# Kernel tuning notes

Measured on AMD Instinct MI355X. Metric: run time of the kernel, lower is better.

The kernel has to match this reference:

```python
import jax, jax.numpy as jnp
import numpy as np

N = 50000      # num nodes
E = 800000     # num edges
DIN = 64       # in_channels
H = 128        # hidden_channels
L = 3          # num GCN layers


def setup_inputs() -> dict:
    key = jax.random.key(0)
    ks = jax.random.split(key, 18)
    x = jax.random.normal(ks[0], (N, DIN), jnp.float32)
    edge_index = jax.random.randint(ks[1], (2, E), 0, N, dtype=jnp.int32)
    s_in = 1.0 / np.sqrt(DIN)
    s_h = 1.0 / np.sqrt(H)
    W_in = jax.random.normal(ks[2], (DIN, H), jnp.float32) * s_in
    b_in = jnp.zeros((H,), jnp.float32)
    Wc = jax.random.normal(ks[3], (L, H, H), jnp.float32) * s_h
    bc = jnp.zeros((L, H), jnp.float32)
    gamma = 1.0 + 0.1 * jax.random.normal(ks[4], (L, H), jnp.float32)
    beta = 0.1 * jax.random.normal(ks[5], (L, H), jnp.float32)
    rmean = 0.1 * jax.random.normal(ks[6], (L, H), jnp.float32)
    rvar = jax.random.uniform(ks[7], (L, H), jnp.float32, 0.5, 1.5)
    W1 = jax.random.normal(ks[8], (H, H // 2), jnp.float32) * s_h
    b1 = jnp.zeros((H // 2,), jnp.float32)
    W2 = jax.random.normal(ks[9], (H // 2, 1), jnp.float32) * (1.0 / np.sqrt(H // 2))
    b2 = jnp.zeros((1,), jnp.float32)
    return dict(x=x, edge_index=edge_index, W_in=W_in, b_in=b_in, Wc=Wc, bc=bc,
                gamma=gamma, beta=beta, rmean=rmean, rvar=rvar,
                W1=W1, b1=b1, W2=W2, b2=b2)


def reference(x, edge_index, W_in, b_in, Wc, bc, gamma, beta, rmean, rvar, W1, b1, W2, b2):
    n = x.shape[0]
    loops = jnp.arange(n, dtype=edge_index.dtype)
    src = jnp.concatenate([edge_index[0], loops])  # [E+N]
    dst = jnp.concatenate([edge_index[1], loops])
    # symmetric GCN normalization with self-loops
    deg = jax.ops.segment_sum(jnp.ones(src.shape[0], jnp.float32), dst, num_segments=n)
    dis = jnp.where(deg > 0, jax.lax.rsqrt(jnp.maximum(deg, 1.0)), 0.0)
    norm = (dis[src] * dis[dst])[:, None]  # [E+N, 1]
    eps = 1e-5

    h = jax.nn.relu(x @ W_in + b_in)  # [N, H]
    for i in range(Wc.shape[0]):
        h_in = h
        hw = h @ Wc[i]                                   # [N, H]
        agg = jax.ops.segment_sum(hw[src] * norm, dst, num_segments=n) + bc[i]
        hbn = (agg - rmean[i]) * jax.lax.rsqrt(rvar[i] + eps) * gamma[i] + beta[i]
        h = jax.nn.relu(hbn)
        if i > 0:
            h = h + h_in  # residual (skipped on first layer, as in source)
        # dropout: eval mode -> identity
    out = jax.nn.relu(h @ W1 + b1) @ W2 + b2  # [N, 1]
    return out.squeeze(-1)
```

## Files before the change

kernel.cpp:

```cpp
#include <hip/hip_runtime.h>


__device__ __forceinline__ void fma4(float4& acc, float s, const float4& v) {
    acc.x = fmaf(s, v.x, acc.x);
    acc.y = fmaf(s, v.y, acc.y);
    acc.z = fmaf(s, v.z, acc.z);
    acc.w = fmaf(s, v.w, acc.w);
}
__device__ __forceinline__ void add4(float4& acc, const float4& v) {
    acc.x += v.x; acc.y += v.y; acc.z += v.z; acc.w += v.w;
}

constexpr int DIN_C = 64;
constexpr int H_C = 128;


__global__ __launch_bounds__(256) void count_deg_kernel(const int* __restrict__ dst,
                                                        int* __restrict__ cnt, int e) {
    int i = blockIdx.x * 256 + threadIdx.x;
    if (i < e) atomicAdd(&cnt[dst[i]], 1);
}

__global__ __launch_bounds__(512) void scan_blocks_kernel(const int* __restrict__ cnt,
                                                          int* __restrict__ excl,
                                                          int* __restrict__ bsums, int n) {
    __shared__ int s[2][512];
    int t = threadIdx.x;
    int i = blockIdx.x * 512 + t;
    int v = (i < n) ? cnt[i] : 0;
    s[0][t] = v;
    __syncthreads();
    int cur = 0;
    for (int off = 1; off < 512; off <<= 1) {
        int x = s[cur][t];
        if (t >= off) x += s[cur][t - off];
        s[cur ^ 1][t] = x;
        cur ^= 1;
        __syncthreads();
    }
    if (i < n) excl[i] = s[cur][t] - v;
    if (t == 511) bsums[blockIdx.x] = s[cur][t];
}

__global__ __launch_bounds__(128) void scan_tops_kernel(const int* __restrict__ bsums,
                                                        int* __restrict__ btops, int nb) {
    __shared__ int s[2][128];
    int t = threadIdx.x;
    int v = (t < nb) ? bsums[t] : 0;
    s[0][t] = v;
    __syncthreads();
    int cur = 0;
    for (int off = 1; off < 128; off <<= 1) {
        int x = s[cur][t];
        if (t >= off) x += s[cur][t - off];
        s[cur ^ 1][t] = x;
        cur ^= 1;
        __syncthreads();
    }
    if (t < nb) btops[t] = s[cur][t] - v;
}

__global__ __launch_bounds__(512) void finalize_nodes_kernel(
        const int* __restrict__ excl, const int* __restrict__ btops,
        const int* __restrict__ cnt, int* __restrict__ row_ptr,
        int* __restrict__ cursor, float* __restrict__ dis, int n, int e) {
    int i = blockIdx.x * 512 + threadIdx.x;
    if (i < n) {
        int rp = excl[i] + btops[blockIdx.x];
        row_ptr[i] = rp;
        cursor[i]  = rp;
        dis[i] = rsqrtf((float)(cnt[i] + 1));
    }
    if (i == 0) row_ptr[n] = e;
}

__global__ __launch_bounds__(256) void fill_csr_kernel(
        const int* __restrict__ src, const int* __restrict__ dst,
        int* __restrict__ cursor, int* __restrict__ csr_src, int e) {
    int i = blockIdx.x * 256 + threadIdx.x;
    if (i < e) {
        int s = src[i], d = dst[i];
        int pos = atomicAdd(&cursor[d], 1);
        csr_src[pos] = s;
    }
}


template <int K, int NC, bool RELU, bool BIAS, bool SCALE>
__global__ __launch_bounds__(256) void gemm_kernel(
        const float* __restrict__ A, const float* __restrict__ W,
        const float* __restrict__ bias, const float* __restrict__ rs,
        float* __restrict__ C, int M) {
    constexpr int CG  = NC / 4;
    constexpr int RG  = 256 / CG;
    constexpr int RPB = RG * 8;
    const int t  = threadIdx.x;
    const int tx = t % CG;
    const int ty = t / CG;
    const int c  = tx * 4;
    const int r0 = blockIdx.x * RPB + ty * 8;

    float4 bv = {0.f, 0.f, 0.f, 0.f};
    if (BIAS) bv = *(const float4*)&bias[c];

    if (r0 + 8 <= M) {
        float4 acc[8];
#pragma unroll
        for (int i = 0; i < 8; ++i) acc[i] = bv;
        const float* Ar = A + (size_t)r0 * K;
#pragma unroll 4
        for (int k0 = 0; k0 < K; k0 += 4) {
            float4 w0 = *(const float4*)&W[(size_t)(k0 + 0) * NC + c];
            float4 w1 = *(const float4*)&W[(size_t)(k0 + 1) * NC + c];
            float4 w2 = *(const float4*)&W[(size_t)(k0 + 2) * NC + c];
            float4 w3 = *(const float4*)&W[(size_t)(k0 + 3) * NC + c];
#pragma unroll
            for (int i = 0; i < 8; ++i) {
                float4 a = *(const float4*)&Ar[(size_t)i * K + k0];
                fma4(acc[i], a.x, w0);
                fma4(acc[i], a.y, w1);
                fma4(acc[i], a.z, w2);
                fma4(acc[i], a.w, w3);
            }
        }
        float* Cr = C + (size_t)r0 * NC + c;
#pragma unroll
        for (int i = 0; i < 8; ++i) {
            float4 v = acc[i];
            if (RELU) {
                v.x = fmaxf(v.x, 0.f); v.y = fmaxf(v.y, 0.f);
                v.z = fmaxf(v.z, 0.f); v.w = fmaxf(v.w, 0.f);
            }
            if (SCALE) {
                float s = rs[r0 + i];
                v.x *= s; v.y *= s; v.z *= s; v.w *= s;
            }
            *(float4*)&Cr[(size_t)i * NC] = v;
        }
    } else {
        for (int i = 0; i < 8; ++i) {
            int r = r0 + i;
            if (r >= M) break;
            float4 acc = bv;
            const float* Ar = A + (size_t)r * K;
            for (int k0 = 0; k0 < K; k0 += 4) {
                float4 a  = *(const float4*)&Ar[k0];
                float4 w0 = *(const float4*)&W[(size_t)(k0 + 0) * NC + c];
                float4 w1 = *(const float4*)&W[(size_t)(k0 + 1) * NC + c];
                float4 w2 = *(const float4*)&W[(size_t)(k0 + 2) * NC + c];
                float4 w3 = *(const float4*)&W[(size_t)(k0 + 3) * NC + c];
                fma4(acc, a.x, w0);
                fma4(acc, a.y, w1);
                fma4(acc, a.z, w2);
                fma4(acc, a.w, w3);
            }
            if (RELU) {
                acc.x = fmaxf(acc.x, 0.f); acc.y = fmaxf(acc.y, 0.f);
                acc.z = fmaxf(acc.z, 0.f); acc.w = fmaxf(acc.w, 0.f);
            }
            if (SCALE) {
                float s = rs[r];
                acc.x *= s; acc.y *= s; acc.z *= s; acc.w *= s;
            }
            *(float4*)&C[(size_t)r * NC + c] = acc;
        }
    }
}


__global__ __launch_bounds__(256) void head_kernel(
        const float* __restrict__ A, const float* __restrict__ W1,
        const float* __restrict__ b1, const float* __restrict__ W2,
        const float* __restrict__ b2, float* __restrict__ out, int M) {
    constexpr int K = 128, NC = 64;
    constexpr int CG  = NC / 4;
    constexpr int RPB = (256 / CG) * 8;
    const int t  = threadIdx.x;
    const int tx = t % CG;
    const int ty = t / CG;
    const int c  = tx * 4;
    const int r0 = blockIdx.x * RPB + ty * 8;

    float4 bv = *(const float4*)&b1[c];
    float4 w2v = *(const float4*)&W2[c];
    float b2v = b2[0];

    float part[8];
    if (r0 + 8 <= M) {
        float4 acc[8];
#pragma unroll
        for (int i = 0; i < 8; ++i) acc[i] = bv;
        const float* Ar = A + (size_t)r0 * K;
#pragma unroll 4
        for (int k0 = 0; k0 < K; k0 += 4) {
            float4 w0 = *(const float4*)&W1[(size_t)(k0 + 0) * NC + c];
            float4 w1 = *(const float4*)&W1[(size_t)(k0 + 1) * NC + c];
            float4 w2 = *(const float4*)&W1[(size_t)(k0 + 2) * NC + c];
            float4 w3 = *(const float4*)&W1[(size_t)(k0 + 3) * NC + c];
#pragma unroll
            for (int i = 0; i < 8; ++i) {
                float4 a = *(const float4*)&Ar[(size_t)i * K + k0];
                fma4(acc[i], a.x, w0);
                fma4(acc[i], a.y, w1);
                fma4(acc[i], a.z, w2);
                fma4(acc[i], a.w, w3);
            }
        }
#pragma unroll
        for (int i = 0; i < 8; ++i) {
            float4 v = acc[i];
            v.x = fmaxf(v.x, 0.f); v.y = fmaxf(v.y, 0.f);
            v.z = fmaxf(v.z, 0.f); v.w = fmaxf(v.w, 0.f);
            part[i] = v.x * w2v.x + v.y * w2v.y + v.z * w2v.z + v.w * w2v.w;
        }
    } else {
#pragma unroll
        for (int i = 0; i < 8; ++i) {
            int r = r0 + i;
            part[i] = 0.f;
            if (r < M) {
                float4 acc = bv;
                const float* Ar = A + (size_t)r * K;
                for (int k0 = 0; k0 < K; k0 += 4) {
                    float4 a  = *(const float4*)&Ar[k0];
                    float4 w0 = *(const float4*)&W1[(size_t)(k0 + 0) * NC + c];
                    float4 w1 = *(const float4*)&W1[(size_t)(k0 + 1) * NC + c];
                    float4 w2 = *(const float4*)&W1[(size_t)(k0 + 2) * NC + c];
                    float4 w3 = *(const float4*)&W1[(size_t)(k0 + 3) * NC + c];
                    fma4(acc, a.x, w0);
                    fma4(acc, a.y, w1);
                    fma4(acc, a.z, w2);
                    fma4(acc, a.w, w3);
                }
                acc.x = fmaxf(acc.x, 0.f); acc.y = fmaxf(acc.y, 0.f);
                acc.z = fmaxf(acc.z, 0.f); acc.w = fmaxf(acc.w, 0.f);
                part[i] = acc.x * w2v.x + acc.y * w2v.y + acc.z * w2v.z + acc.w * w2v.w;
            }
        }
    }
#pragma unroll
    for (int i = 0; i < 8; ++i) {
        float v = part[i];
        v += __shfl_xor(v, 1);
        v += __shfl_xor(v, 2);
        v += __shfl_xor(v, 4);
        v += __shfl_xor(v, 8);
        part[i] = v;
    }
    if (tx == 0) {
#pragma unroll
        for (int i = 0; i < 8; ++i) {
            int r = r0 + i;
            if (r < M) out[r] = part[i] + b2v;
        }
    }
}


__global__ __launch_bounds__(256) void agg_bn_kernel(
        const float* __restrict__ hwp, const int* __restrict__ row_ptr,
        const int* __restrict__ csr_src, const float* __restrict__ dis,
        const float* __restrict__ bc, const float* __restrict__ gamma_,
        const float* __restrict__ beta_, const float* __restrict__ rmean,
        const float* __restrict__ rvar,
        const float* __restrict__ h_in, float* __restrict__ h_out,
        int n, int residual) {
    int wid  = (blockIdx.x * 256 + threadIdx.x) >> 6;
    int lane = threadIdx.x & 63;
    if (wid >= n) return;
    const int half = lane >> 5;
    const int f    = (lane & 31) * 4;

    float4 a0 = {0.f, 0.f, 0.f, 0.f};
    float4 a1 = {0.f, 0.f, 0.f, 0.f};
    float4 a2 = {0.f, 0.f, 0.f, 0.f};
    float4 a3 = {0.f, 0.f, 0.f, 0.f};
    if (half == 0) a0 = *(const float4*)(hwp + (size_t)wid * H_C + f);

    const int beg = row_ptr[wid], end = row_ptr[wid + 1];
    int e = beg + half;
    for (; e + 6 < end; e += 8) {
        int s0 = csr_src[e];
        int s1 = csr_src[e + 2];
        int s2 = csr_src[e + 4];
        int s3 = csr_src[e + 6];
        float4 r0 = *(const float4*)(hwp + (size_t)s0 * H_C + f);
        float4 r1 = *(const float4*)(hwp + (size_t)s1 * H_C + f);
        float4 r2 = *(const float4*)(hwp + (size_t)s2 * H_C + f);
        float4 r3 = *(const float4*)(hwp + (size_t)s3 * H_C + f);
        add4(a0, r0);
        add4(a1, r1);
        add4(a2, r2);
        add4(a3, r3);
    }
    for (; e + 2 < end; e += 4) {
        int s0 = csr_src[e];
        int s1 = csr_src[e + 2];
        float4 r0 = *(const float4*)(hwp + (size_t)s0 * H_C + f);
        float4 r1 = *(const float4*)(hwp + (size_t)s1 * H_C + f);
        add4(a0, r0);
        add4(a1, r1);
    }
    if (e < end) {
        int s = csr_src[e];
        float4 r = *(const float4*)(hwp + (size_t)s * H_C + f);
        add4(a0, r);
    }
    add4(a0, a2);
    add4(a1, a3);
    add4(a0, a1);
    a0.x += __shfl_xor(a0.x, 32);
    a0.y += __shfl_xor(a0.y, 32);
    a0.z += __shfl_xor(a0.z, 32);
    a0.w += __shfl_xor(a0.w, 32);

    if (half == 0) {
        const float eps = 1e-5f;
        float dd = dis[wid];
        float4 b4 = *(const float4*)&bc[f];
        float4 g4 = *(const float4*)&gamma_[f];
        float4 be4 = *(const float4*)&beta_[f];
        float4 m4 = *(const float4*)&rmean[f];
        float4 v4 = *(const float4*)&rvar[f];
        float4 o;
        o.x = fmaf((fmaf(dd, a0.x, b4.x) - m4.x) * rsqrtf(v4.x + eps), g4.x, be4.x);
        o.y = fmaf((fmaf(dd, a0.y, b4.y) - m4.y) * rsqrtf(v4.y + eps), g4.y, be4.y);
        o.z = fmaf((fmaf(dd, a0.z, b4.z) - m4.z) * rsqrtf(v4.z + eps), g4.z, be4.z);
        o.w = fmaf((fmaf(dd, a0.w, b4.w) - m4.w) * rsqrtf(v4.w + eps), g4.w, be4.w);
        o.x = fmaxf(o.x, 0.f); o.y = fmaxf(o.y, 0.f);
        o.z = fmaxf(o.z, 0.f); o.w = fmaxf(o.w, 0.f);
        if (residual) {
            float4 r = *(const float4*)(h_in + (size_t)wid * H_C + f);
            add4(o, r);
        }
        *(float4*)(h_out + (size_t)wid * H_C + f) = o;
    }
}


extern "C" void kernel_launch(void* const* d_in, const int* in_sizes, int n_in,
                              void* d_out, int out_size, void* d_ws, size_t ws_size,
                              hipStream_t stream) {
    const float* x      = (const float*)d_in[0];
    const int*   ei     = (const int*)  d_in[1];
    const float* W_in   = (const float*)d_in[2];
    const float* b_in   = (const float*)d_in[3];
    const float* Wc     = (const float*)d_in[4];
    const float* bc     = (const float*)d_in[5];
    const float* gamma_ = (const float*)d_in[6];
    const float* beta_  = (const float*)d_in[7];
    const float* rmean  = (const float*)d_in[8];
    const float* rvar   = (const float*)d_in[9];
    const float* W1     = (const float*)d_in[10];
    const float* b1     = (const float*)d_in[11];
    const float* W2     = (const float*)d_in[12];
    const float* b2     = (const float*)d_in[13];
    float* out = (float*)d_out;

    const int M = in_sizes[0] / DIN_C;
    const int E = in_sizes[1] / 2;
    const int* src = ei;
    const int* dst = ei + E;

    size_t off = 0;
    auto alloc = [&](size_t bytes) {
        void* p = (char*)d_ws + off;
        off += (bytes + 255) & ~(size_t)255;
        return p;
    };
    int*   cnt      = (int*)  alloc((size_t)M * 4);
    int*   excl     = (int*)  alloc((size_t)M * 4);
    int*   bsums    = (int*)  alloc(512);
    int*   btops    = (int*)  alloc(512);
    int*   row_ptr  = (int*)  alloc((size_t)(M + 1) * 4);
    int*   cursor   = (int*)  alloc((size_t)M * 4);
    float* dis      = (float*)alloc((size_t)M * 4);
    int*   csr_src  = (int*)  alloc((size_t)E * 4);
    float* hA       = (float*)alloc((size_t)M * H_C * 4);
    float* hB       = (float*)alloc((size_t)M * H_C * 4);
    float* hw       = (float*)alloc((size_t)M * H_C * 4);

    const int NB = (M + 511) / 512;

    hipMemsetAsync(cnt, 0, (size_t)M * 4, stream);
    count_deg_kernel<<<(E + 255) / 256, 256, 0, stream>>>(dst, cnt, E);
    scan_blocks_kernel<<<NB, 512, 0, stream>>>(cnt, excl, bsums, M);
    scan_tops_kernel<<<1, 128, 0, stream>>>(bsums, btops, NB);
    finalize_nodes_kernel<<<NB, 512, 0, stream>>>(excl, btops, cnt, row_ptr, cursor, dis, M, E);
    fill_csr_kernel<<<(E + 255) / 256, 256, 0, stream>>>(src, dst, cursor, csr_src, E);

    {
        constexpr int RPB = (256 / (H_C / 4)) * 8;
        gemm_kernel<DIN_C, H_C, true, true, false><<<(M + RPB - 1) / RPB, 256, 0, stream>>>(
            x, W_in, b_in, nullptr, hA, M);
    }

    float* cur = hA;
    float* nxt = hB;
    for (int layer = 0; layer < 3; ++layer) {
        constexpr int RPB = (256 / (H_C / 4)) * 8;
        gemm_kernel<H_C, H_C, false, false, true><<<(M + RPB - 1) / RPB, 256, 0, stream>>>(
            cur, Wc + (size_t)layer * H_C * H_C, nullptr, dis, hw, M);
        agg_bn_kernel<<<(M * 64 + 255) / 256, 256, 0, stream>>>(
            hw, row_ptr, csr_src, dis,
            bc + (size_t)layer * H_C, gamma_ + (size_t)layer * H_C,
            beta_ + (size_t)layer * H_C, rmean + (size_t)layer * H_C,
            rvar + (size_t)layer * H_C,
            cur, nxt, M, layer > 0 ? 1 : 0);
        float* tmp = cur; cur = nxt; nxt = tmp;
    }

    {
        constexpr int RPB = (256 / (64 / 4)) * 8;
        head_kernel<<<(M + RPB - 1) / RPB, 256, 0, stream>>>(
            cur, W1, b1, W2, b2, out, M);
    }
}
```

Measured before the change: 565.7 us.

## Replace FP32 FMA GEMMs with split-bf16 MFMA matrix-core GEMMs

Rewrites the node-feature GEMMs (input projection and per-layer transform) to use MFMA 16x16x32 bf16 instructions. Both operands are split into hi and lo bf16 parts, and three MFMAs per tile recover near-FP32 accuracy. A new kernel pre-splits and transposes the weights each call. This replaces the scalar FMA inner loops with matrix-core work, at the cost of conversion overhead, one extra launch, and uncoalesced scalar stores of the output.

```diff
diff --git a/kernel.cpp b/kernel.cpp
--- a/kernel.cpp
+++ b/kernel.cpp
@@ -1,5 +1,9 @@
 #include <hip/hip_runtime.h>
 
+
+typedef unsigned short ushort_t;
+typedef __attribute__((ext_vector_type(8))) short bf16x8;
+typedef __attribute__((ext_vector_type(4))) float f32x4;
 
 __device__ __forceinline__ void fma4(float4& acc, float s, const float4& v) {
     acc.x = fmaf(s, v.x, acc.x);
@@ -9,6 +13,16 @@
 }
 __device__ __forceinline__ void add4(float4& acc, const float4& v) {
     acc.x += v.x; acc.y += v.y; acc.z += v.z; acc.w += v.w;
+}
+
+__device__ __forceinline__ ushort_t f2bf(float x) {
+    union { float f; unsigned u; } v; v.f = x;
+    unsigned r = v.u + 0x7FFFu + ((v.u >> 16) & 1u);
+    return (ushort_t)(r >> 16);
+}
+__device__ __forceinline__ float bf2f(ushort_t h) {
+    union { unsigned u; float f; } v; v.u = ((unsigned)h) << 16;
+    return v.f;
 }
 
 constexpr int DIN_C = 64;
@@ -86,83 +100,92 @@
 }
 
 
-template <int K, int NC, bool RELU, bool BIAS, bool SCALE>
-__global__ __launch_bounds__(256) void gemm_kernel(
-        const float* __restrict__ A, const float* __restrict__ W,
-        const float* __restrict__ bias, const float* __restrict__ rs,
-        float* __restrict__ C, int M) {
-    constexpr int CG  = NC / 4;
-    constexpr int RG  = 256 / CG;
-    constexpr int RPB = RG * 8;
-    const int t  = threadIdx.x;
-    const int tx = t % CG;
-    const int ty = t / CG;
-    const int c  = tx * 4;
-    const int r0 = blockIdx.x * RPB + ty * 8;
-
-    float4 bv = {0.f, 0.f, 0.f, 0.f};
-    if (BIAS) bv = *(const float4*)&bias[c];
-
-    if (r0 + 8 <= M) {
-        float4 acc[8];
-#pragma unroll
-        for (int i = 0; i < 8; ++i) acc[i] = bv;
-        const float* Ar = A + (size_t)r0 * K;
-#pragma unroll 4
-        for (int k0 = 0; k0 < K; k0 += 4) {
-            float4 w0 = *(const float4*)&W[(size_t)(k0 + 0) * NC + c];
-            float4 w1 = *(const float4*)&W[(size_t)(k0 + 1) * NC + c];
-            float4 w2 = *(const float4*)&W[(size_t)(k0 + 2) * NC + c];
-            float4 w3 = *(const float4*)&W[(size_t)(k0 + 3) * NC + c];
-#pragma unroll
-            for (int i = 0; i < 8; ++i) {
-                float4 a = *(const float4*)&Ar[(size_t)i * K + k0];
-                fma4(acc[i], a.x, w0);
-                fma4(acc[i], a.y, w1);
-                fma4(acc[i], a.z, w2);
-                fma4(acc[i], a.w, w3);
+__global__ __launch_bounds__(256) void wsplit_kernel(
+        const float* __restrict__ Wc, const float* __restrict__ W_in,
+        ushort_t* __restrict__ lt_hi, ushort_t* __restrict__ lt_lo,
+        ushort_t* __restrict__ it_hi, ushort_t* __restrict__ it_lo) {
+    int i = blockIdx.x * 256 + threadIdx.x;
+    if (i < 3 * 128 * 128) {
+        int m = i >> 14, rem = i & 16383;
+        int k = rem >> 7, n = rem & 127;
+        float v = Wc[i];
+        ushort_t h = f2bf(v);
+        ushort_t l = f2bf(v - bf2f(h));
+        lt_hi[(m << 14) + n * 128 + k] = h;
+        lt_lo[(m << 14) + n * 128 + k] = l;
+    } else {
+        int j = i - 3 * 128 * 128;
+        if (j < 64 * 128) {
+            int k = j >> 7, n = j & 127;
+            float v = W_in[j];
+            ushort_t h = f2bf(v);
+            ushort_t l = f2bf(v - bf2f(h));
+            it_hi[n * 64 + k] = h;
+            it_lo[n * 64 + k] = l;
+        }
+    }
+}
+
+
+template <int KSTEPS, bool RELU, bool BIAS, bool SCALE>
+__global__ __launch_bounds__(256) void gemm_mfma_kernel(
+        const float* __restrict__ A, const ushort_t* __restrict__ wt_hi,
+        const ushort_t* __restrict__ wt_lo, const float* __restrict__ bias,
+        const float* __restrict__ rs, float* __restrict__ C, int M) {
+    constexpr int K = KSTEPS * 32;
+    const int tid  = threadIdx.x;
+    const int wid  = tid >> 6;
+    const int lane = tid & 63;
+    const int lo16 = lane & 15;
+    const int hi4  = lane >> 4;
+    const int r0   = blockIdx.x * 64 + wid * 16;
+
+    f32x4 acc[8];
+#pragma unroll
+    for (int nt = 0; nt < 8; ++nt) {
+        float b = BIAS ? bias[nt * 16 + lo16] : 0.f;
+        acc[nt] = (f32x4){b, b, b, b};
+    }
+
+    int ar = r0 + lo16;
+    if (ar > M - 1) ar = M - 1;
+    const float* Arow = A + (size_t)ar * K;
+
+#pragma unroll
+    for (int kb = 0; kb < KSTEPS; ++kb) {
+        const float4* ap = (const float4*)(Arow + kb * 32 + hi4 * 8);
+        float4 a0 = ap[0], a1 = ap[1];
+        float av[8] = {a0.x, a0.y, a0.z, a0.w, a1.x, a1.y, a1.z, a1.w};
+        bf16x8 afh, afl;
+#pragma unroll
+        for (int j = 0; j < 8; ++j) {
+            ushort_t h = f2bf(av[j]);
+            afh[j] = (short)h;
+            afl[j] = (short)f2bf(av[j] - bf2f(h));
+        }
+        const int kof = kb * 32 + hi4 * 8;
+#pragma unroll
+        for (int nt = 0; nt < 8; ++nt) {
+            const size_t boff = (size_t)(nt * 16 + lo16) * K + kof;
+            bf16x8 bfh = *(const bf16x8*)(wt_hi + boff);
+            bf16x8 bfl = *(const bf16x8*)(wt_lo + boff);
+            acc[nt] = __builtin_amdgcn_mfma_f32_16x16x32_bf16(afh, bfh, acc[nt], 0, 0, 0);
+            acc[nt] = __builtin_amdgcn_mfma_f32_16x16x32_bf16(afh, bfl, acc[nt], 0, 0, 0);
+            acc[nt] = __builtin_amdgcn_mfma_f32_16x16x32_bf16(afl, bfh, acc[nt], 0, 0, 0);
+        }
+    }
+
+#pragma unroll
+    for (int reg = 0; reg < 4; ++reg) {
+        int r = r0 + hi4 * 4 + reg;
+        if (r < M) {
+            float s = SCALE ? rs[r] : 1.f;
+#pragma unroll
+            for (int nt = 0; nt < 8; ++nt) {
+                float v = acc[nt][reg];
+                if (RELU) v = fmaxf(v, 0.f);
+                C[(size_t)r * 128 + nt * 16 + lo16] = SCALE ? v * s : v;
             }
-        }
-        float* Cr = C + (size_t)r0 * NC + c;
-#pragma unroll
-        for (int i = 0; i < 8; ++i) {
-            float4 v = acc[i];
-            if (RELU) {
-                v.x = fmaxf(v.x, 0.f); v.y = fmaxf(v.y, 0.f);
-                v.z = fmaxf(v.z, 0.f); v.w = fmaxf(v.w, 0.f);
-            }
-            if (SCALE) {
-                float s = rs[r0 + i];
-                v.x *= s; v.y *= s; v.z *= s; v.w *= s;
-            }
-            *(float4*)&Cr[(size_t)i * NC] = v;
-        }
-    } else {
-        for (int i = 0; i < 8; ++i) {
-            int r = r0 + i;
-            if (r >= M) break;
-            float4 acc = bv;
-            const float* Ar = A + (size_t)r * K;
-            for (int k0 = 0; k0 < K; k0 += 4) {
-                float4 a  = *(const float4*)&Ar[k0];
-                float4 w0 = *(const float4*)&W[(size_t)(k0 + 0) * NC + c];
-                float4 w1 = *(const float4*)&W[(size_t)(k0 + 1) * NC + c];
-                float4 w2 = *(const float4*)&W[(size_t)(k0 + 2) * NC + c];
-                float4 w3 = *(const float4*)&W[(size_t)(k0 + 3) * NC + c];
-                fma4(acc, a.x, w0);
-                fma4(acc, a.y, w1);
-                fma4(acc, a.z, w2);
-                fma4(acc, a.w, w3);
-            }
-            if (RELU) {
-                acc.x = fmaxf(acc.x, 0.f); acc.y = fmaxf(acc.y, 0.f);
-                acc.z = fmaxf(acc.z, 0.f); acc.w = fmaxf(acc.w, 0.f);
-            }
-            if (SCALE) {
-                float s = rs[r];
-                acc.x *= s; acc.y *= s; acc.z *= s; acc.w *= s;
-            }
-            *(float4*)&C[(size_t)r * NC + c] = acc;
         }
     }
 }
@@ -368,19 +391,29 @@
         off += (bytes + 255) & ~(size_t)255;
         return p;
     };
-    int*   cnt      = (int*)  alloc((size_t)M * 4);
-    int*   excl     = (int*)  alloc((size_t)M * 4);
-    int*   bsums    = (int*)  alloc(512);
-    int*   btops    = (int*)  alloc(512);
-    int*   row_ptr  = (int*)  alloc((size_t)(M + 1) * 4);
-    int*   cursor   = (int*)  alloc((size_t)M * 4);
-    float* dis      = (float*)alloc((size_t)M * 4);
-    int*   csr_src  = (int*)  alloc((size_t)E * 4);
-    float* hA       = (float*)alloc((size_t)M * H_C * 4);
-    float* hB       = (float*)alloc((size_t)M * H_C * 4);
-    float* hw       = (float*)alloc((size_t)M * H_C * 4);
+    int*      cnt      = (int*)     alloc((size_t)M * 4);
+    int*      excl     = (int*)     alloc((size_t)M * 4);
+    int*      bsums    = (int*)     alloc(512);
+    int*      btops    = (int*)     alloc(512);
+    int*      row_ptr  = (int*)     alloc((size_t)(M + 1) * 4);
+    int*      cursor   = (int*)     alloc((size_t)M * 4);
+    float*    dis      = (float*)   alloc((size_t)M * 4);
+    int*      csr_src  = (int*)     alloc((size_t)E * 4);
+    ushort_t* lt_hi    = (ushort_t*)alloc((size_t)3 * 128 * 128 * 2);
+    ushort_t* lt_lo    = (ushort_t*)alloc((size_t)3 * 128 * 128 * 2);
+    ushort_t* it_hi    = (ushort_t*)alloc((size_t)128 * 64 * 2);
+    ushort_t* it_lo    = (ushort_t*)alloc((size_t)128 * 64 * 2);
+    float*    hA       = (float*)   alloc((size_t)M * H_C * 4);
+    float*    hB       = (float*)   alloc((size_t)M * H_C * 4);
+    float*    hw       = (float*)   alloc((size_t)M * H_C * 4);
 
     const int NB = (M + 511) / 512;
+
+    {
+        const int total = 3 * 128 * 128 + 64 * 128;
+        wsplit_kernel<<<(total + 255) / 256, 256, 0, stream>>>(
+            Wc, W_in, lt_hi, lt_lo, it_hi, it_lo);
+    }
 
     hipMemsetAsync(cnt, 0, (size_t)M * 4, stream);
     count_deg_kernel<<<(E + 255) / 256, 256, 0, stream>>>(dst, cnt, E);
@@ -389,18 +422,17 @@
     finalize_nodes_kernel<<<NB, 512, 0, stream>>>(excl, btops, cnt, row_ptr, cursor, dis, M, E);
     fill_csr_kernel<<<(E + 255) / 256, 256, 0, stream>>>(src, dst, cursor, csr_src, E);
 
-    {
-        constexpr int RPB = (256 / (H_C / 4)) * 8;
-        gemm_kernel<DIN_C, H_C, true, true, false><<<(M + RPB - 1) / RPB, 256, 0, stream>>>(
-            x, W_in, b_in, nullptr, hA, M);
-    }
+    const int GEMM_GRID = (M + 63) / 64;
+
+    gemm_mfma_kernel<2, true, true, false><<<GEMM_GRID, 256, 0, stream>>>(
+        x, it_hi, it_lo, b_in, nullptr, hA, M);
 
     float* cur = hA;
     float* nxt = hB;
     for (int layer = 0; layer < 3; ++layer) {
-        constexpr int RPB = (256 / (H_C / 4)) * 8;
-        gemm_kernel<H_C, H_C, false, false, true><<<(M + RPB - 1) / RPB, 256, 0, stream>>>(
-            cur, Wc + (size_t)layer * H_C * H_C, nullptr, dis, hw, M);
+        gemm_mfma_kernel<4, false, false, true><<<GEMM_GRID, 256, 0, stream>>>(
+            cur, lt_hi + (size_t)layer * 16384, lt_lo + (size_t)layer * 16384,
+            nullptr, dis, hw, M);
         agg_bn_kernel<<<(M * 64 + 255) / 256, 256, 0, stream>>>(
             hw, row_ptr, csr_src, dis,
             bc + (size_t)layer * H_C, gamma_ + (size_t)layer * H_C,
```

After: 525.8 us. -7.1%, faster.
